# Performance work log

Hardware: AMD Instinct MI355X
Metric: run time of the kernel (lower is better)

## Reference

```python
import jax, jax.numpy as jnp
import numpy as np

EMBED_DIM = 768
NUM_HEADS = 12
DILATION_RATES = [1, 2, 4]
SEGMENT_LENGTHS = [2048, 4096, 8192]
LN_EPS = 1e-5
CAUSAL = False


def _dilated_attention(q, k, v, causal=False):
    # q, k, v: (b, N, h, d)
    b, N, h, d = q.shape
    g = len(DILATION_RATES)
    gs = h // g
    scale = 1.0 / jnp.sqrt(jnp.asarray(d, q.dtype))
    out = jnp.zeros_like(q)
    for i, (r, s) in enumerate(zip(DILATION_RATES, SEGMENT_LENGTHS)):
        n = N // s
        offset = i % r
        hmin, hmax = i * gs, (i + 1) * gs
        # strided gather: (b, n, s_eff, gs, d)
        qi = q.reshape(b, n, s, h, d)[:, :, offset::r, hmin:hmax, :]
        ki = k.reshape(b, n, s, h, d)[:, :, offset::r, hmin:hmax, :]
        vi = v.reshape(b, n, s, h, d)[:, :, offset::r, hmin:hmax, :]
        scores = jnp.einsum('bnqhd,bnkhd->bnhqk', qi, ki) * scale
        if causal:
            s_eff = qi.shape[2]
            mask = jnp.tril(jnp.ones((s_eff, s_eff), dtype=bool))
            scores = jnp.where(mask, scores, jnp.asarray(-jnp.inf, scores.dtype))
        p = jax.nn.softmax(scores, axis=-1)
        x = jnp.einsum('bnhqk,bnkhd->bnqhd', p, vi)
        # original normalization: divide by sum over (segment, position) dims
        x = x / x.sum(axis=(1, 2), keepdims=True)
        out = (out.reshape(b, n, s, h, d)
                  .at[:, :, offset::r, hmin:hmax, :].add(x)
                  .reshape(b, N, h, d))
    return out / g


def setup_inputs() -> dict:
    key = jax.random.key(0)
    ks = jax.random.split(key, 13)
    b, N, E = 2, 8192, EMBED_DIM
    sd = 1.0 / np.sqrt(E)
    return {
        'query': jax.random.normal(ks[0], (b, N, E), jnp.float32),
        'key': jax.random.normal(ks[1], (b, N, E), jnp.float32),
        'value': jax.random.normal(ks[2], (b, N, E), jnp.float32),
        'Wq': jax.random.normal(ks[3], (E, E), jnp.float32) * sd,
        'bq': jnp.zeros((E,), jnp.float32),
        'Wk': jax.random.normal(ks[4], (E, E), jnp.float32) * sd,
        'bk': jnp.zeros((E,), jnp.float32),
        'Wv': jax.random.normal(ks[5], (E, E), jnp.float32) * sd,
        'bv': jnp.zeros((E,), jnp.float32),
        'Wo': jax.random.normal(ks[6], (E, E), jnp.float32) * sd,
        'bo': jnp.zeros((E,), jnp.float32),
        'ln_w': jnp.ones((E,), jnp.float32),
        'ln_b': jnp.zeros((E,), jnp.float32),
    }


def reference(query, key, value, Wq, bq, Wk, bk, Wv, bv, Wo, bo, ln_w, ln_b):
    b, N, E = query.shape
    h = NUM_HEADS
    d = E // h
    q = (query @ Wq + bq).reshape(b, N, h, d)
    k = (key @ Wk + bk).reshape(b, N, h, d)
    v = (value @ Wv + bv).reshape(b, N, h, d)
    x = _dilated_attention(q, k, v, causal=CAUSAL).reshape(b, N, E)
    mu = x.mean(axis=-1, keepdims=True)
    var = x.var(axis=-1, keepdims=True)
    x = (x - mu) / jnp.sqrt(var + LN_EPS) * ln_w + ln_b
    return x @ Wo + bo
```

## Files before the change

kernel.cpp:

```cpp
#include <hip/hip_runtime.h>

typedef __attribute__((ext_vector_type(4))) float f32x4;
typedef __attribute__((ext_vector_type(4))) unsigned int u32x4;
typedef __attribute__((ext_vector_type(8))) _Float16 half8;
typedef __attribute__((ext_vector_type(2))) _Float16 half2v;

__device__ inline f32x4 mfma_fp16(half8 a, half8 b, f32x4 c) {
  return __builtin_amdgcn_mfma_f32_16x16x32_f16(a, b, c, 0, 0, 0);
}

__device__ inline int kva(int row, int colbyte) {
  return ((row * 128 + colbyte) ^ ((row & 7) << 4)) >> 1;
}

__device__ inline void gload16(const _Float16* g, _Float16* l) {
  __builtin_amdgcn_global_load_lds(
      (const __attribute__((address_space(1))) void*)g,
      (__attribute__((address_space(3))) void*)l, 16, 0, 0);
}

__global__ __launch_bounds__(256) void wsplit4_kernel(
    const float* __restrict__ Wq, const float* __restrict__ Wk,
    const float* __restrict__ Wv, const float* __restrict__ Wo,
    _Float16* __restrict__ Whi, _Float16* __restrict__ Wlo) {
  int w = blockIdx.y;
  const float* W = (w == 0) ? Wq : (w == 1) ? Wk : (w == 2) ? Wv : Wo;
  int i = blockIdx.x * 256 + threadIdx.x;
  int k = i / 768, n = i % 768;
  float v = W[i];
  _Float16 h = (_Float16)v;
  Whi[w * 589824 + n * 768 + k] = h;
  Wlo[w * 589824 + n * 768 + k] = (_Float16)(v - (float)h);
}

__device__ inline void asplit_body(const float* __restrict__ A,
                                   _Float16* __restrict__ Ahi,
                                   _Float16* __restrict__ Alo, int i) {
  f32x4 x0 = *(const f32x4*)(A + i);
  f32x4 x1 = *(const f32x4*)(A + i + 4);
  half8 vh, vl;
#pragma unroll
  for (int j = 0; j < 4; ++j) {
    _Float16 h0 = (_Float16)x0[j];
    vh[j] = h0; vl[j] = (_Float16)(x0[j] - (float)h0);
    _Float16 h1 = (_Float16)x1[j];
    vh[4 + j] = h1; vl[4 + j] = (_Float16)(x1[j] - (float)h1);
  }
  *(half8*)(Ahi + i) = vh;
  *(half8*)(Alo + i) = vl;
}

__global__ __launch_bounds__(256) void asplit_kernel(const float* __restrict__ A,
                                                     _Float16* __restrict__ Ahi,
                                                     _Float16* __restrict__ Alo) {
  asplit_body(A, Ahi, Alo, (blockIdx.x * 256 + threadIdx.x) * 8);
}

__global__ __launch_bounds__(256) void asplit3_kernel(
    const float* __restrict__ Aq, const float* __restrict__ Ak,
    const float* __restrict__ Av,
    _Float16* __restrict__ Aqh, _Float16* __restrict__ Aql,
    _Float16* __restrict__ Akh, _Float16* __restrict__ Akl,
    _Float16* __restrict__ Avh, _Float16* __restrict__ Avl) {
  int w = blockIdx.y;
  const float* A = (w == 0) ? Aq : (w == 1) ? Ak : Av;
  _Float16* H = (w == 0) ? Aqh : (w == 1) ? Akh : Avh;
  _Float16* L = (w == 0) ? Aql : (w == 1) ? Akl : Avl;
  asplit_body(A, H, L, (blockIdx.x * 256 + threadIdx.x) * 8);
}

__device__ inline int vt_base(int b, int h) {
  int base = b * 3670016;
  if (h < 4)      base += h * 524288;
  else if (h < 8) base += 2097152 + (h - 4) * 262144;
  else            base += 3145728 + (h - 8) * 131072;
  return base;
}

__device__ __forceinline__ void gemm3_core(
    const _Float16* __restrict__ Ahi, const _Float16* __restrict__ Alo,
    const _Float16* __restrict__ Bhi, const _Float16* __restrict__ Blo,
    const float* __restrict__ bias, _Float16* __restrict__ Chi,
    _Float16* __restrict__ Clo, int mode, int m0, int n0,
    _Float16* Ah, _Float16* Al, _Float16* Bh, _Float16* Bl) {
  int tid = threadIdx.x;
  int lane = tid & 63, wid = tid >> 6;
  int wm = wid >> 1, wn = wid & 1;
  int lg = lane >> 4, lc = lane & 15;

  f32x4 acc[2][4] = {};

  size_t sA[2], sB[2];
  int ldst[2];
#pragma unroll
  for (int c = 0; c < 2; ++c) {
    int idxv = c * 512 + tid;
    int m = idxv >> 3;
    int ke = ((idxv & 7) << 3) ^ ((m & 7) << 3);
    sA[c] = (size_t)(m0 + m) * 768 + ke;
    sB[c] = (size_t)(n0 + m) * 768 + ke;
    ldst[c] = (c * 512 + wid * 64) * 8;
  }

  for (int k0 = 0; k0 < 768; k0 += 64) {
    __syncthreads();
#pragma unroll
    for (int c = 0; c < 2; ++c) {
      gload16(Ahi + sA[c] + k0, Ah + ldst[c]);
      gload16(Alo + sA[c] + k0, Al + ldst[c]);
      gload16(Bhi + sB[c] + k0, Bh + ldst[c]);
      gload16(Blo + sB[c] + k0, Bl + ldst[c]);
    }
    __syncthreads();

#pragma unroll
    for (int ks = 0; ks < 2; ++ks) {
      half8 ah[2], al[2], bh[4], bl[4];
#pragma unroll
      for (int mt = 0; mt < 2; ++mt) {
        int ro = kva(wm * 32 + mt * 16 + lc, ks * 64 + (lg << 4));
        ah[mt] = *(half8*)(&Ah[ro]);
        al[mt] = *(half8*)(&Al[ro]);
      }
#pragma unroll
      for (int nf = 0; nf < 4; ++nf) {
        int ro = kva(wn * 64 + nf * 16 + lc, ks * 64 + (lg << 4));
        bh[nf] = *(half8*)(&Bh[ro]);
        bl[nf] = *(half8*)(&Bl[ro]);
      }
#pragma unroll
      for (int mt = 0; mt < 2; ++mt)
#pragma unroll
        for (int nf = 0; nf < 4; ++nf) {
          acc[mt][nf] = mfma_fp16(al[mt], bh[nf], acc[mt][nf]);
          acc[mt][nf] = mfma_fp16(ah[mt], bl[nf], acc[mt][nf]);
          acc[mt][nf] = mfma_fp16(ah[mt], bh[nf], acc[mt][nf]);
        }
    }
  }

#pragma unroll
  for (int mt = 0; mt < 2; ++mt)
#pragma unroll
    for (int nf = 0; nf < 4; ++nf) {
      int col = n0 + wn * 64 + nf * 16 + lc;
      int row0 = m0 + wm * 32 + mt * 16 + (lg << 2);
      float bv = bias[col];
#pragma unroll
      for (int rr = 0; rr < 4; ++rr) {
        int row = row0 + rr;
        float v = acc[mt][nf][rr] + bv;
        _Float16 h = (_Float16)v;
        _Float16 l = (_Float16)(v - (float)h);
        if (mode == 0) {
          Chi[(size_t)row * 768 + col] = h;
          Clo[(size_t)row * 768 + col] = l;
        } else {
          int b = row >> 13, pos = row & 8191;
          int hh = col >> 6, d = col & 63;
          int g = hh >> 2;
          int rdil = 1 << g;
          if ((pos & (rdil - 1)) == g) {
            int t = (pos - g) >> g;
            int Ng = 8192 >> g;
            Chi[vt_base(b, hh) + d * Ng + t] = h;
            Clo[vt_base(b, hh) + d * Ng + t] = l;
          }
        }
      }
    }
}

__global__ __launch_bounds__(512, 2) void gemm3_kernel(
    const _Float16* __restrict__ Ahi, const _Float16* __restrict__ Alo,
    const _Float16* __restrict__ Bhi, const _Float16* __restrict__ Blo,
    const float* __restrict__ bias,
    _Float16* __restrict__ Chi, _Float16* __restrict__ Clo, int mode) {
  __shared__ _Float16 Ah[128 * 64], Al[128 * 64], Bh[128 * 64], Bl[128 * 64];
  gemm3_core(Ahi, Alo, Bhi, Blo, bias, Chi, Clo, mode,
             blockIdx.y * 128, blockIdx.x * 128, Ah, Al, Bh, Bl);
}

__global__ __launch_bounds__(512, 2) void gemm3b_kernel(
    const _Float16* __restrict__ Aqh, const _Float16* __restrict__ Aql,
    const _Float16* __restrict__ Akh, const _Float16* __restrict__ Akl,
    const _Float16* __restrict__ Avh, const _Float16* __restrict__ Avl,
    const _Float16* __restrict__ Wsh, const _Float16* __restrict__ Wsl,
    const float* __restrict__ bq, const float* __restrict__ bk,
    const float* __restrict__ bv,
    _Float16* __restrict__ Qhb, _Float16* __restrict__ Qlb,
    _Float16* __restrict__ Khb, _Float16* __restrict__ Klb,
    _Float16* __restrict__ Vth, _Float16* __restrict__ Vtl) {
  __shared__ _Float16 Ah[128 * 64], Al[128 * 64], Bh[128 * 64], Bl[128 * 64];
  int orig = blockIdx.x;
  int wg = (orig & 7) * 288 + (orig >> 3);
  int sec = wg / 768, rem = wg % 768;
  int m0 = (rem / 6) * 128, n0 = (rem % 6) * 128;
  const _Float16* Ahi = (sec == 0) ? Aqh : (sec == 1) ? Akh : Avh;
  const _Float16* Alo = (sec == 0) ? Aql : (sec == 1) ? Akl : Avl;
  const float* bias = (sec == 0) ? bq : (sec == 1) ? bk : bv;
  _Float16* Chi = (sec == 0) ? Qhb : (sec == 1) ? Khb : Vth;
  _Float16* Clo = (sec == 0) ? Qlb : (sec == 1) ? Klb : Vtl;
  gemm3_core(Ahi, Alo, Wsh + sec * 589824, Wsl + sec * 589824, bias,
             Chi, Clo, (sec == 2) ? 1 : 0, m0, n0, Ah, Al, Bh, Bl);
}

__global__ __launch_bounds__(256, 4) void gemm1_kernel(
    const _Float16* __restrict__ A, const _Float16* __restrict__ Bt,
    const float* __restrict__ bias, float* __restrict__ C) {
  __shared__ _Float16 As[128 * 64];
  __shared__ _Float16 Bs[128 * 64];
  int orig = blockIdx.x;
  int wg = (orig & 7) * 96 + (orig >> 3);
  int m0 = (wg / 6) * 128, n0 = (wg % 6) * 128;
  int tid = threadIdx.x;
  int lane = tid & 63, wid = tid >> 6;
  int wm = wid >> 1, wn = wid & 1;
  int lg = lane >> 4, lc = lane & 15;

  f32x4 acc[4][4] = {};

  size_t sA[4], sB[4];
  int ldst[4];
#pragma unroll
  for (int c = 0; c < 4; ++c) {
    int idxv = c * 256 + tid;
    int m = idxv >> 3;
    int ke = ((idxv & 7) << 3) ^ ((m & 7) << 3);
    sA[c] = (size_t)(m0 + m) * 768 + ke;
    sB[c] = (size_t)(n0 + m) * 768 + ke;
    ldst[c] = (c * 256 + wid * 64) * 8;
  }

  for (int k0 = 0; k0 < 768; k0 += 64) {
    __syncthreads();
#pragma unroll
    for (int c = 0; c < 4; ++c) {
      gload16(A + sA[c] + k0, As + ldst[c]);
      gload16(Bt + sB[c] + k0, Bs + ldst[c]);
    }
    __syncthreads();
#pragma unroll
    for (int ks = 0; ks < 2; ++ks) {
      half8 af[4], bf[4];
#pragma unroll
      for (int mt = 0; mt < 4; ++mt)
        af[mt] = *(half8*)(&As[kva(wm * 64 + mt * 16 + lc, ks * 64 + (lg << 4))]);
#pragma unroll
      for (int nf = 0; nf < 4; ++nf)
        bf[nf] = *(half8*)(&Bs[kva(wn * 64 + nf * 16 + lc, ks * 64 + (lg << 4))]);
#pragma unroll
      for (int mt = 0; mt < 4; ++mt)
#pragma unroll
        for (int nf = 0; nf < 4; ++nf)
          acc[mt][nf] = mfma_fp16(af[mt], bf[nf], acc[mt][nf]);
    }
  }

#pragma unroll
  for (int mt = 0; mt < 4; ++mt)
#pragma unroll
    for (int nf = 0; nf < 4; ++nf) {
      int col = n0 + wn * 64 + nf * 16 + lc;
      int row0 = m0 + wm * 64 + mt * 16 + (lg << 2);
      float bv = bias[col];
#pragma unroll
      for (int rr = 0; rr < 4; ++rr)
        C[(size_t)(row0 + rr) * 768 + col] = acc[mt][nf][rr] + bv;
    }
}

__global__ __launch_bounds__(256, 4) void attn_kernel(
    const _Float16* __restrict__ Qh, const _Float16* __restrict__ Ql,
    const _Float16* __restrict__ Kh, const _Float16* __restrict__ Kl,
    const _Float16* __restrict__ Vth, const _Float16* __restrict__ Vtl,
    _Float16* __restrict__ Xh, float* __restrict__ partial) {
  __shared__ _Float16 Ksh[64 * 64], Ksl[64 * 64];
  __shared__ _Float16 Vsh[64 * 64], Vsl[64 * 64];
  __shared__ float wred[4][64];

  int bid = blockIdx.x;
  int xcd = bid & 7, idx = bid >> 3;
  int u_glob = xcd * 7 + (idx >> 4);
  int qblk = idx & 15;
  int g = (u_glob < 32) ? 0 : (u_glob < 48) ? 1 : 2;
  int u = (g == 0) ? u_glob : (g == 1) ? u_glob - 32 : u_glob - 48;
  int nsegs = 4 >> g;
  int b = u / (nsegs * 4), rem = u % (nsegs * 4);
  int nseg = rem >> 2, hg = rem & 3;
  int head = g * 4 + hg;
  int s = 2048 << g, r = 1 << g, off = g;
  int Ng = 8192 >> g;
  int tbase = nseg * 2048;
  int vbase = vt_base(b, head);

  int tid = threadIdx.x, lane = tid & 63, wid = tid >> 6;
  int lg = lane >> 4, lc = lane & 15;

  int q0 = qblk * 128 + wid * 32;
  half8 qAh[2], qAl[2], qBh[2], qBl[2];
  {
    int posA = nseg * s + off + (q0 + lc) * r;
    int posB = nseg * s + off + (q0 + 16 + lc) * r;
    size_t roA = (size_t)(b * 8192 + posA) * 768 + head * 64;
    size_t roB = (size_t)(b * 8192 + posB) * 768 + head * 64;
#pragma unroll
    for (int ks = 0; ks < 2; ++ks) {
      qAh[ks] = *(const half8*)(Qh + roA + ks * 32 + (lg << 3));
      qAl[ks] = *(const half8*)(Ql + roA + ks * 32 + (lg << 3));
      qBh[ks] = *(const half8*)(Qh + roB + ks * 32 + (lg << 3));
      qBl[ks] = *(const half8*)(Ql + roB + ks * 32 + (lg << 3));
    }
  }

  int krl = (lane >> 3);
  int ke = (((lane & 7) ^ krl) << 3);
  size_t kro[2], vro[2];
  int ldk[2];
#pragma unroll
  for (int c = 0; c < 2; ++c) {
    int kr = c * 32 + wid * 8 + krl;
    kro[c] = (size_t)(b * 8192 + nseg * s + off + kr * r) * 768 + head * 64 + ke;
    vro[c] = (size_t)vbase + (size_t)kr * Ng + tbase + ke;
    ldk[c] = c * 2048 + wid * 512;
  }
  const size_t kstep = (size_t)64 * r * 768;

  f32x4 accA[4] = {};
  f32x4 accB[4] = {};
  float lsumA = 0.f, lsumB = 0.f;

  const int sl0 = ((lane & 16) << 1) + lc;
  const int sl1 = sl0 + 16;
  const bool hiSel = (lane & 32) != 0;

  for (int kt = 0; kt < 32; ++kt) {
    __syncthreads();
#pragma unroll
    for (int c = 0; c < 2; ++c) {
      gload16(Kh + kro[c], Ksh + ldk[c]);
      gload16(Kl + kro[c], Ksl + ldk[c]);
      gload16(Vth + vro[c], Vsh + ldk[c]);
      gload16(Vtl + vro[c], Vsl + ldk[c]);
      kro[c] += kstep;
      vro[c] += 64;
    }
    __syncthreads();

    unsigned int pkA[4][2], pkB[4][2];
#pragma unroll
    for (int nf = 0; nf < 4; ++nf) {
      half8 kh[2], kl[2];
#pragma unroll
      for (int ks = 0; ks < 2; ++ks) {
        int ro = kva(nf * 16 + lc, ks * 64 + (lg << 4));
        kh[ks] = *(half8*)(&Ksh[ro]);
        kl[ks] = *(half8*)(&Ksl[ro]);
      }
      f32x4 tA = {}, tB = {};
#pragma unroll
      for (int ks = 0; ks < 2; ++ks) {
        tA = mfma_fp16(kl[ks], qAh[ks], tA);
        tA = mfma_fp16(kh[ks], qAl[ks], tA);
        tB = mfma_fp16(kl[ks], qBh[ks], tB);
        tB = mfma_fp16(kh[ks], qBl[ks], tB);
      }
#pragma unroll
      for (int ks = 0; ks < 2; ++ks) {
        tA = mfma_fp16(kh[ks], qAh[ks], tA);
        tB = mfma_fp16(kh[ks], qBh[ks], tB);
      }
      _Float16 hA[4], hB[4];
#pragma unroll
      for (int rr = 0; rr < 4; ++rr) {
        float pA = __expf(tA[rr] * 0.125f);
        float pB = __expf(tB[rr] * 0.125f);
        hA[rr] = (_Float16)pA; lsumA += (float)hA[rr];
        hB[rr] = (_Float16)pB; lsumB += (float)hB[rr];
      }
      half2v a01 = {hA[0], hA[1]}, a23 = {hA[2], hA[3]};
      half2v b01 = {hB[0], hB[1]}, b23 = {hB[2], hB[3]};
      pkA[nf][0] = __builtin_bit_cast(unsigned int, a01);
      pkA[nf][1] = __builtin_bit_cast(unsigned int, a23);
      pkB[nf][0] = __builtin_bit_cast(unsigned int, b01);
      pkB[nf][1] = __builtin_bit_cast(unsigned int, b23);
    }

#pragma unroll
    for (int ks2 = 0; ks2 < 2; ++ks2) {
      int nfA = 2 * ks2, nfB = 2 * ks2 + 1;
      unsigned int aA0 = __shfl(pkA[nfA][0], sl0, 64);
      unsigned int aB0 = __shfl(pkA[nfB][0], sl0, 64);
      unsigned int aA1 = __shfl(pkA[nfA][1], sl0, 64);
      unsigned int aB1 = __shfl(pkA[nfB][1], sl0, 64);
      unsigned int aA2 = __shfl(pkA[nfA][0], sl1, 64);
      unsigned int aB2 = __shfl(pkA[nfB][0], sl1, 64);
      unsigned int aA3 = __shfl(pkA[nfA][1], sl1, 64);
      unsigned int aB3 = __shfl(pkA[nfB][1], sl1, 64);
      u32x4 pwA;
      pwA[0] = hiSel ? aB0 : aA0;
      pwA[1] = hiSel ? aB1 : aA1;
      pwA[2] = hiSel ? aB2 : aA2;
      pwA[3] = hiSel ? aB3 : aA3;
      half8 paA = __builtin_bit_cast(half8, pwA);

      unsigned int bA0 = __shfl(pkB[nfA][0], sl0, 64);
      unsigned int bB0 = __shfl(pkB[nfB][0], sl0, 64);
      unsigned int bA1 = __shfl(pkB[nfA][1], sl0, 64);
      unsigned int bB1 = __shfl(pkB[nfB][1], sl0, 64);
      unsigned int bA2 = __shfl(pkB[nfA][0], sl1, 64);
      unsigned int bB2 = __shfl(pkB[nfB][0], sl1, 64);
      unsigned int bA3 = __shfl(pkB[nfA][1], sl1, 64);
      unsigned int bB3 = __shfl(pkB[nfB][1], sl1, 64);
      u32x4 pwB;
      pwB[0] = hiSel ? bB0 : bA0;
      pwB[1] = hiSel ? bB1 : bA1;
      pwB[2] = hiSel ? bB2 : bA2;
      pwB[3] = hiSel ? bB3 : bA3;
      half8 paB = __builtin_bit_cast(half8, pwB);

#pragma unroll
      for (int nf = 0; nf < 4; ++nf) {
        int ro = kva(nf * 16 + lc, ks2 * 64 + (lg << 4));
        half8 vh = *(half8*)(&Vsh[ro]);
        half8 vl = *(half8*)(&Vsl[ro]);
        accA[nf] = mfma_fp16(paA, vl, accA[nf]);
        accA[nf] = mfma_fp16(paA, vh, accA[nf]);
        accB[nf] = mfma_fp16(paB, vl, accB[nf]);
        accB[nf] = mfma_fp16(paB, vh, accB[nf]);
      }
    }
  }

  lsumA += __shfl_xor(lsumA, 16, 64);
  lsumA += __shfl_xor(lsumA, 32, 64);
  lsumB += __shfl_xor(lsumB, 16, 64);
  lsumB += __shfl_xor(lsumB, 32, 64);
  float invA = 1.0f / lsumA;
  float invB = 1.0f / lsumB;

  float cs[4] = {};
#pragma unroll
  for (int rr = 0; rr < 4; ++rr) {
    int qi = ((lane >> 4) & 3) * 4 + rr;
    float invqA = __shfl(invA, (lane & 48) + qi, 64);
    float invqB = __shfl(invB, (lane & 48) + qi, 64);
    int posA = nseg * s + off + (q0 + qi) * r;
    int posB = nseg * s + off + (q0 + 16 + qi) * r;
    _Float16* xrA = Xh + (size_t)(b * 8192 + posA) * 768 + head * 64;
    _Float16* xrB = Xh + (size_t)(b * 8192 + posB) * 768 + head * 64;
#pragma unroll
    for (int nf = 0; nf < 4; ++nf) {
      _Float16 hxA = (_Float16)(accA[nf][rr] * invqA);
      _Float16 hxB = (_Float16)(accB[nf][rr] * invqB);
      xrA[nf * 16 + lc] = hxA;
      xrB[nf * 16 + lc] = hxB;
      cs[nf] += (float)hxA + (float)hxB;
    }
  }
#pragma unroll
  for (int nf = 0; nf < 4; ++nf) {
    cs[nf] += __shfl_xor(cs[nf], 16, 64);
    cs[nf] += __shfl_xor(cs[nf], 32, 64);
    if (lane < 16) wred[wid][nf * 16 + lc] = cs[nf];
  }
  __syncthreads();
  if (tid < 64) {
    float w4 = wred[0][tid] + wred[1][tid] + wred[2][tid] + wred[3][tid];
    int slot = ((b * 12 + head) * 64 + nseg * 16 + qblk);
    partial[slot * 64 + tid] = w4;
  }
}

__global__ __launch_bounds__(256) void colsum2_kernel(const float* __restrict__ partial,
                                                      float* __restrict__ divbuf) {
  int i = blockIdx.x * 256 + threadIdx.x;
  int b = i / 768, e = i % 768;
  int h = e >> 6, d = e & 63;
  int g = h >> 2;
  int nslots = 64 >> g;
  const float* src = partial + (size_t)((b * 12 + h) * 64) * 64 + d;
  float sacc = 0.f;
  for (int c = 0; c < nslots; ++c) sacc += src[c * 64];
  divbuf[i] = sacc;
}

__global__ __launch_bounds__(256) void ln_kernel(const _Float16* __restrict__ Xh,
                                                 _Float16* __restrict__ Xln,
                                                 const float* __restrict__ divbuf,
                                                 const float* __restrict__ ln_w,
                                                 const float* __restrict__ ln_b) {
  int wid = threadIdx.x >> 6, lane = threadIdx.x & 63;
  int row = blockIdx.x * 4 + wid;
  int b = row >> 13, pos = row & 8191;
  float x[12];
  float s1 = 0.f, s2 = 0.f;
#pragma unroll
  for (int j = 0; j < 12; ++j) {
    int e = lane + 64 * j;
    int g = j >> 2;
    bool wr = (g == 0) || (g == 1 && (pos & 1) == 1) || (g == 2 && (pos & 3) == 2);
    float v = 0.f;
    if (wr) v = (float)Xh[(size_t)row * 768 + e] / (divbuf[b * 768 + e] * 3.0f);
    x[j] = v;
    s1 += v;
    s2 += v * v;
  }
#pragma unroll
  for (int msk = 1; msk < 64; msk <<= 1) {
    s1 += __shfl_xor(s1, msk, 64);
    s2 += __shfl_xor(s2, msk, 64);
  }
  float mean = s1 * (1.0f / 768.0f);
  float var = s2 * (1.0f / 768.0f) - mean * mean;
  float inv = rsqrtf(var + 1e-5f);
#pragma unroll
  for (int j = 0; j < 12; ++j) {
    int e = lane + 64 * j;
    Xln[(size_t)row * 768 + e] = (_Float16)((x[j] - mean) * inv * ln_w[e] + ln_b[e]);
  }
}

extern "C" void kernel_launch(void* const* d_in, const int* in_sizes, int n_in,
                              void* d_out, int out_size, void* d_ws, size_t ws_size,
                              hipStream_t stream) {
  const float* query = (const float*)d_in[0];
  const float* key   = (const float*)d_in[1];
  const float* value = (const float*)d_in[2];
  const float* Wq = (const float*)d_in[3];
  const float* bq = (const float*)d_in[4];
  const float* Wk = (const float*)d_in[5];
  const float* bk = (const float*)d_in[6];
  const float* Wv = (const float*)d_in[7];
  const float* bv = (const float*)d_in[8];
  const float* Wo = (const float*)d_in[9];
  const float* bo = (const float*)d_in[10];
  const float* ln_w = (const float*)d_in[11];
  const float* ln_b = (const float*)d_in[12];

  char* ws = (char*)d_ws;
  _Float16* Wsh = (_Float16*)ws; ws += (size_t)4 * 589824 * 2;
  _Float16* Wsl = (_Float16*)ws; ws += (size_t)4 * 589824 * 2;
  _Float16* Qhb = (_Float16*)ws; ws += (size_t)16384 * 768 * 2;
  _Float16* Qlb = (_Float16*)ws; ws += (size_t)16384 * 768 * 2;
  _Float16* Khb = (_Float16*)ws; ws += (size_t)16384 * 768 * 2;
  _Float16* Klb = (_Float16*)ws; ws += (size_t)16384 * 768 * 2;
  _Float16* Vth = (_Float16*)ws; ws += (size_t)7340032 * 2;
  _Float16* Vtl = (_Float16*)ws; ws += (size_t)7340032 * 2;
  char* Xregion = ws; ws += (size_t)16384 * 768 * 4;
  float* partial = (float*)ws; ws += (size_t)24 * 64 * 64 * 4;
  float* divbuf = (float*)ws; ws += 2 * 768 * 4;

  _Float16* Xh  = (_Float16*)Xregion;
  _Float16* Xln = Xh + (size_t)16384 * 768;
  _Float16* Aqh = (_Float16*)Xregion;
  _Float16* Aql = Aqh + (size_t)16384 * 768;

  size_t base_bytes = (size_t)(ws - (char*)d_ws);
  size_t extra = (size_t)4 * 16384 * 768 * 2;
  bool batched = ws_size >= base_bytes + extra;

  wsplit4_kernel<<<dim3(2304, 4), 256, 0, stream>>>(Wq, Wk, Wv, Wo, Wsh, Wsl);

  dim3 ggrid(6, 128);
  if (batched) {
    _Float16* Akh = (_Float16*)ws; ws += (size_t)16384 * 768 * 2;
    _Float16* Akl = (_Float16*)ws; ws += (size_t)16384 * 768 * 2;
    _Float16* Avh = (_Float16*)ws; ws += (size_t)16384 * 768 * 2;
    _Float16* Avl = (_Float16*)ws; ws += (size_t)16384 * 768 * 2;
    asplit3_kernel<<<dim3(6144, 3), 256, 0, stream>>>(query, key, value,
        Aqh, Aql, Akh, Akl, Avh, Avl);
    gemm3b_kernel<<<2304, 512, 0, stream>>>(
        Aqh, Aql, Akh, Akl, Avh, Avl, Wsh, Wsl, bq, bk, bv,
        Qhb, Qlb, Khb, Klb, Vth, Vtl);
  } else {
    asplit_kernel<<<6144, 256, 0, stream>>>(query, Aqh, Aql);
    gemm3_kernel<<<ggrid, 512, 0, stream>>>(Aqh, Aql, Wsh, Wsl, bq, Qhb, Qlb, 0);
    asplit_kernel<<<6144, 256, 0, stream>>>(key, Aqh, Aql);
    gemm3_kernel<<<ggrid, 512, 0, stream>>>(Aqh, Aql, Wsh + 589824, Wsl + 589824, bk, Khb, Klb, 0);
    asplit_kernel<<<6144, 256, 0, stream>>>(value, Aqh, Aql);
    gemm3_kernel<<<ggrid, 512, 0, stream>>>(Aqh, Aql, Wsh + 2 * 589824, Wsl + 2 * 589824, bv, Vth, Vtl, 1);
  }

  attn_kernel<<<896, 256, 0, stream>>>(Qhb, Qlb, Khb, Klb, Vth, Vtl, Xh, partial);

  colsum2_kernel<<<6, 256, 0, stream>>>(partial, divbuf);
  ln_kernel<<<4096, 256, 0, stream>>>(Xh, Xln, divbuf, ln_w, ln_b);

  gemm1_kernel<<<768, 256, 0, stream>>>(Xln, Wsh + 3 * 589824, bo, (float*)d_out);
}
```

Baseline: 617.8 us.

## Fuse fp32-to-fp16 hi/lo activation split into the QKV projection GEMM

Removes the separate asplit kernels and has the QKV GEMM read raw fp32 query/key/value. Each tile is split into hi/lo fp16 halves in registers and written straight into the swizzled LDS tiles. This avoids writing and re-reading the large intermediate fp16 activation buffers and one kernel launch, and drops the non-batched fallback path. The cost is synchronous register-staged global loads for A instead of async global_load_lds, and redundant conversion work, since each A tile is re-split by all six N-column blocks.

```diff
diff --git a/kernel.cpp b/kernel.cpp
--- a/kernel.cpp
+++ b/kernel.cpp
@@ -33,42 +33,6 @@
   Wlo[w * 589824 + n * 768 + k] = (_Float16)(v - (float)h);
 }
 
-__device__ inline void asplit_body(const float* __restrict__ A,
-                                   _Float16* __restrict__ Ahi,
-                                   _Float16* __restrict__ Alo, int i) {
-  f32x4 x0 = *(const f32x4*)(A + i);
-  f32x4 x1 = *(const f32x4*)(A + i + 4);
-  half8 vh, vl;
-#pragma unroll
-  for (int j = 0; j < 4; ++j) {
-    _Float16 h0 = (_Float16)x0[j];
-    vh[j] = h0; vl[j] = (_Float16)(x0[j] - (float)h0);
-    _Float16 h1 = (_Float16)x1[j];
-    vh[4 + j] = h1; vl[4 + j] = (_Float16)(x1[j] - (float)h1);
-  }
-  *(half8*)(Ahi + i) = vh;
-  *(half8*)(Alo + i) = vl;
-}
-
-__global__ __launch_bounds__(256) void asplit_kernel(const float* __restrict__ A,
-                                                     _Float16* __restrict__ Ahi,
-                                                     _Float16* __restrict__ Alo) {
-  asplit_body(A, Ahi, Alo, (blockIdx.x * 256 + threadIdx.x) * 8);
-}
-
-__global__ __launch_bounds__(256) void asplit3_kernel(
-    const float* __restrict__ Aq, const float* __restrict__ Ak,
-    const float* __restrict__ Av,
-    _Float16* __restrict__ Aqh, _Float16* __restrict__ Aql,
-    _Float16* __restrict__ Akh, _Float16* __restrict__ Akl,
-    _Float16* __restrict__ Avh, _Float16* __restrict__ Avl) {
-  int w = blockIdx.y;
-  const float* A = (w == 0) ? Aq : (w == 1) ? Ak : Av;
-  _Float16* H = (w == 0) ? Aqh : (w == 1) ? Akh : Avh;
-  _Float16* L = (w == 0) ? Aql : (w == 1) ? Akl : Avl;
-  asplit_body(A, H, L, (blockIdx.x * 256 + threadIdx.x) * 8);
-}
-
 __device__ inline int vt_base(int b, int h) {
   int base = b * 3670016;
   if (h < 4)      base += h * 524288;
@@ -78,7 +42,7 @@
 }
 
 __device__ __forceinline__ void gemm3_core(
-    const _Float16* __restrict__ Ahi, const _Float16* __restrict__ Alo,
+    const float* __restrict__ Araw,
     const _Float16* __restrict__ Bhi, const _Float16* __restrict__ Blo,
     const float* __restrict__ bias, _Float16* __restrict__ Chi,
     _Float16* __restrict__ Clo, int mode, int m0, int n0,
@@ -90,15 +54,16 @@
 
   f32x4 acc[2][4] = {};
 
-  size_t sA[2], sB[2];
-  int ldst[2];
+  size_t aoff[2], sB[2];
+  int lA[2], ldst[2];
 #pragma unroll
   for (int c = 0; c < 2; ++c) {
     int idxv = c * 512 + tid;
-    int m = idxv >> 3;
-    int ke = ((idxv & 7) << 3) ^ ((m & 7) << 3);
-    sA[c] = (size_t)(m0 + m) * 768 + ke;
-    sB[c] = (size_t)(n0 + m) * 768 + ke;
+    int mrow = idxv >> 3, ch = idxv & 7;
+    aoff[c] = (size_t)(m0 + mrow) * 768 + ch * 8;
+    lA[c] = kva(mrow, ch << 4);
+    int ke = (ch << 3) ^ ((mrow & 7) << 3);
+    sB[c] = (size_t)(n0 + mrow) * 768 + ke;
     ldst[c] = (c * 512 + wid * 64) * 8;
   }
 
@@ -106,8 +71,18 @@
     __syncthreads();
 #pragma unroll
     for (int c = 0; c < 2; ++c) {
-      gload16(Ahi + sA[c] + k0, Ah + ldst[c]);
-      gload16(Alo + sA[c] + k0, Al + ldst[c]);
+      f32x4 x0 = *(const f32x4*)(Araw + aoff[c] + k0);
+      f32x4 x1 = *(const f32x4*)(Araw + aoff[c] + k0 + 4);
+      half8 vh, vl;
+#pragma unroll
+      for (int j = 0; j < 4; ++j) {
+        _Float16 h0 = (_Float16)x0[j];
+        vh[j] = h0; vl[j] = (_Float16)(x0[j] - (float)h0);
+        _Float16 h1 = (_Float16)x1[j];
+        vh[4 + j] = h1; vl[4 + j] = (_Float16)(x1[j] - (float)h1);
+      }
+      *(half8*)(&Ah[lA[c]]) = vh;
+      *(half8*)(&Al[lA[c]]) = vl;
       gload16(Bhi + sB[c] + k0, Bh + ldst[c]);
       gload16(Blo + sB[c] + k0, Bl + ldst[c]);
     }
@@ -171,20 +146,9 @@
     }
 }
 
-__global__ __launch_bounds__(512, 2) void gemm3_kernel(
-    const _Float16* __restrict__ Ahi, const _Float16* __restrict__ Alo,
-    const _Float16* __restrict__ Bhi, const _Float16* __restrict__ Blo,
-    const float* __restrict__ bias,
-    _Float16* __restrict__ Chi, _Float16* __restrict__ Clo, int mode) {
-  __shared__ _Float16 Ah[128 * 64], Al[128 * 64], Bh[128 * 64], Bl[128 * 64];
-  gemm3_core(Ahi, Alo, Bhi, Blo, bias, Chi, Clo, mode,
-             blockIdx.y * 128, blockIdx.x * 128, Ah, Al, Bh, Bl);
-}
-
 __global__ __launch_bounds__(512, 2) void gemm3b_kernel(
-    const _Float16* __restrict__ Aqh, const _Float16* __restrict__ Aql,
-    const _Float16* __restrict__ Akh, const _Float16* __restrict__ Akl,
-    const _Float16* __restrict__ Avh, const _Float16* __restrict__ Avl,
+    const float* __restrict__ query, const float* __restrict__ key,
+    const float* __restrict__ value,
     const _Float16* __restrict__ Wsh, const _Float16* __restrict__ Wsl,
     const float* __restrict__ bq, const float* __restrict__ bk,
     const float* __restrict__ bv,
@@ -196,12 +160,11 @@
   int wg = (orig & 7) * 288 + (orig >> 3);
   int sec = wg / 768, rem = wg % 768;
   int m0 = (rem / 6) * 128, n0 = (rem % 6) * 128;
-  const _Float16* Ahi = (sec == 0) ? Aqh : (sec == 1) ? Akh : Avh;
-  const _Float16* Alo = (sec == 0) ? Aql : (sec == 1) ? Akl : Avl;
+  const float* Araw = (sec == 0) ? query : (sec == 1) ? key : value;
   const float* bias = (sec == 0) ? bq : (sec == 1) ? bk : bv;
   _Float16* Chi = (sec == 0) ? Qhb : (sec == 1) ? Khb : Vth;
   _Float16* Clo = (sec == 0) ? Qlb : (sec == 1) ? Klb : Vtl;
-  gemm3_core(Ahi, Alo, Wsh + sec * 589824, Wsl + sec * 589824, bias,
+  gemm3_core(Araw, Wsh + sec * 589824, Wsl + sec * 589824, bias,
              Chi, Clo, (sec == 2) ? 1 : 0, m0, n0, Ah, Al, Bh, Bl);
 }
 
@@ -547,40 +510,16 @@
   _Float16* Klb = (_Float16*)ws; ws += (size_t)16384 * 768 * 2;
   _Float16* Vth = (_Float16*)ws; ws += (size_t)7340032 * 2;
   _Float16* Vtl = (_Float16*)ws; ws += (size_t)7340032 * 2;
-  char* Xregion = ws; ws += (size_t)16384 * 768 * 4;
+  _Float16* Xh  = (_Float16*)ws; ws += (size_t)16384 * 768 * 2;
+  _Float16* Xln = (_Float16*)ws; ws += (size_t)16384 * 768 * 2;
   float* partial = (float*)ws; ws += (size_t)24 * 64 * 64 * 4;
   float* divbuf = (float*)ws; ws += 2 * 768 * 4;
 
-  _Float16* Xh  = (_Float16*)Xregion;
-  _Float16* Xln = Xh + (size_t)16384 * 768;
-  _Float16* Aqh = (_Float16*)Xregion;
-  _Float16* Aql = Aqh + (size_t)16384 * 768;
-
-  size_t base_bytes = (size_t)(ws - (char*)d_ws);
-  size_t extra = (size_t)4 * 16384 * 768 * 2;
-  bool batched = ws_size >= base_bytes + extra;
-
   wsplit4_kernel<<<dim3(2304, 4), 256, 0, stream>>>(Wq, Wk, Wv, Wo, Wsh, Wsl);
 
-  dim3 ggrid(6, 128);
-  if (batched) {
-    _Float16* Akh = (_Float16*)ws; ws += (size_t)16384 * 768 * 2;
-    _Float16* Akl = (_Float16*)ws; ws += (size_t)16384 * 768 * 2;
-    _Float16* Avh = (_Float16*)ws; ws += (size_t)16384 * 768 * 2;
-    _Float16* Avl = (_Float16*)ws; ws += (size_t)16384 * 768 * 2;
-    asplit3_kernel<<<dim3(6144, 3), 256, 0, stream>>>(query, key, value,
-        Aqh, Aql, Akh, Akl, Avh, Avl);
-    gemm3b_kernel<<<2304, 512, 0, stream>>>(
-        Aqh, Aql, Akh, Akl, Avh, Avl, Wsh, Wsl, bq, bk, bv,
-        Qhb, Qlb, Khb, Klb, Vth, Vtl);
-  } else {
-    asplit_kernel<<<6144, 256, 0, stream>>>(query, Aqh, Aql);
-    gemm3_kernel<<<ggrid, 512, 0, stream>>>(Aqh, Aql, Wsh, Wsl, bq, Qhb, Qlb, 0);
-    asplit_kernel<<<6144, 256, 0, stream>>>(key, Aqh, Aql);
-    gemm3_kernel<<<ggrid, 512, 0, stream>>>(Aqh, Aql, Wsh + 589824, Wsl + 589824, bk, Khb, Klb, 0);
-    asplit_kernel<<<6144, 256, 0, stream>>>(value, Aqh, Aql);
-    gemm3_kernel<<<ggrid, 512, 0, stream>>>(Aqh, Aql, Wsh + 2 * 589824, Wsl + 2 * 589824, bv, Vth, Vtl, 1);
-  }
+  gemm3b_kernel<<<2304, 512, 0, stream>>>(
+      query, key, value, Wsh, Wsl, bq, bk, bv,
+      Qhb, Qlb, Khb, Klb, Vth, Vtl);
 
   attn_kernel<<<896, 256, 0, stream>>>(Qhb, Qlb, Khb, Klb, Vth, Vtl, Xh, partial);
 
```

New measurement: 537.6 us. 1.15x faster.
